# Optimization experiments

Measured on AMD Instinct MI355X. Metric: run time of the kernel, lower is better.

## Reference

```python
import jax, jax.numpy as jnp
import numpy as np

T = 6   # n_tokens_per_window
H = 4   # num_heads


def setup_inputs() -> dict:
    key = jax.random.key(0)
    ks = jax.random.split(key, 13)
    B, N, E = 64, 512, 256
    s = 0.05  # small init scale for weight matrices (stability)
    return {
        "x": jax.random.normal(ks[0], (B, N * T, E), jnp.float32),
        "mask": jax.random.randint(ks[1], (B, N * T), 0, 2, jnp.int32),
        "query": jax.random.normal(ks[2], (E,), jnp.float32),  # classification_query (1,1,E) squeezed
        "in_proj_w": jax.random.normal(ks[3], (3 * E, E), jnp.float32) * s,
        "in_proj_b": jnp.zeros((3 * E,), jnp.float32),
        "out_w": jax.random.normal(ks[4], (E, E), jnp.float32) * s,
        "out_b": jnp.zeros((E,), jnp.float32),
        "ln_g": jnp.ones((E,), jnp.float32),
        "ln_b": jnp.zeros((E,), jnp.float32),
        "w1": jax.random.normal(ks[5], (E // 2, E), jnp.float32) * s,
        "b1": jnp.zeros((E // 2,), jnp.float32),
        "w2": jax.random.normal(ks[6], (1, E // 2), jnp.float32) * s,
        "b2": jnp.zeros((1,), jnp.float32),
    }


def reference(x, mask, query, in_proj_w, in_proj_b, out_w, out_b,
              ln_g, ln_b, w1, b1, w2, b2):
    B, S, E = x.shape
    N = S // T
    BN = B * N
    hd = E // H

    xr = x.reshape(BN, T, E)                      # (BN, T, E)
    mr = mask.reshape(BN, T).astype(bool)         # token validity per window
    valid = mr.any(axis=1)                        # (BN,) window validity

    # --- single-query multi-head attention (torch MHA, eval mode) ---
    Wq, Wk, Wv = in_proj_w[:E], in_proj_w[E:2 * E], in_proj_w[2 * E:]
    bq, bk, bv = in_proj_b[:E], in_proj_b[E:2 * E], in_proj_b[2 * E:]
    q = (query @ Wq.T + bq).reshape(H, hd)        # shared learnable query
    k = (xr @ Wk.T + bk).reshape(BN, T, H, hd)
    v = (xr @ Wv.T + bv).reshape(BN, T, H, hd)

    scores = jnp.einsum('hd,bthd->bht', q, k) / np.float32(np.sqrt(hd))
    scores = jnp.where(mr[:, None, :], scores, jnp.float32(-1e9))  # key_padding_mask
    attw = jax.nn.softmax(scores, axis=-1)        # (BN, H, T)
    attn = jnp.einsum('bht,bthd->bhd', attw, v).reshape(BN, E)
    attn = attn @ out_w.T + out_b                 # out_proj

    # --- classifier: LayerNorm -> Linear -> GELU -> Linear ---
    mu = attn.mean(-1, keepdims=True)
    var = ((attn - mu) ** 2).mean(-1, keepdims=True)
    h = (attn - mu) / jnp.sqrt(var + 1e-5) * ln_g + ln_b
    h = jax.nn.gelu(h @ w1.T + b1, approximate=False)
    logits = h @ w2.T + b2                        # (BN, 1)

    # zero-fill fully masked windows (torch: logits[~valid_windows_mask] = 0)
    logits = jnp.where(valid[:, None], logits, jnp.float32(0.0))
    return logits.reshape(B, N)                   # n_classes == 1 -> squeeze
```

## Files before the change

kernel.cpp:

```cpp
#include <hip/hip_runtime.h>
#include <math.h>

#define TT 6
#define HH 4
#define EE 256
#define RB 16
#define PR 8
#define NTHREADS 256

typedef __attribute__((ext_vector_type(8))) short bf16x8;
typedef __attribute__((ext_vector_type(4))) float f32x4;

__device__ __forceinline__ unsigned short f2b(float f) {
    union { float f; unsigned u; } v; v.f = f;
    unsigned u = v.u + 0x7fffu + ((v.u >> 16) & 1u);
    return (unsigned short)(u >> 16);
}
__device__ __forceinline__ float b2f(unsigned short s) {
    union { unsigned u; float f; } v; v.u = ((unsigned)s) << 16;
    return v.f;
}

#define SWT_OFF 0
#define SB_OFF  8192
#define Q_OFF   8208
#define WVB_OFF 9232
#define OWB_OFF 140304
#define W1B_OFF 271376

__global__ void setup_q(const float* __restrict__ query,
                        const float* __restrict__ in_proj_w,
                        const float* __restrict__ in_proj_b,
                        unsigned char* __restrict__ ws)
{
    __shared__ float qs[EE];
    float* qv = (float*)(ws + Q_OFF);
    float* sb = (float*)(ws + SB_OFF);
    const int tid = threadIdx.x;
    float acc = in_proj_b[tid];
    const float* row = in_proj_w + (size_t)tid * EE;
    for (int e = 0; e < EE; e += 4) {
        float4 w = *(const float4*)(row + e);
        float4 q = *(const float4*)(query + e);
        acc += w.x * q.x + w.y * q.y + w.z * q.z + w.w * q.w;
    }
    qs[tid] = acc;
    qv[tid] = acc;
    __syncthreads();
    if (tid < HH) {
        float a = 0.f;
        for (int d = 0; d < 64; ++d) a += qs[tid * 64 + d] * in_proj_b[EE + tid * 64 + d];
        sb[tid] = a;
    }
}

__global__ void setup_cast(const float* __restrict__ in_proj_w,
                           const float* __restrict__ out_w,
                           const float* __restrict__ w1,
                           unsigned char* __restrict__ ws)
{
    unsigned short* swt = (unsigned short*)(ws + SWT_OFF);
    const float*    qv  = (const float*)(ws + Q_OFF);
    unsigned short* wvb = (unsigned short*)(ws + WVB_OFF);
    unsigned short* owb = (unsigned short*)(ws + OWB_OFF);
    unsigned short* w1b = (unsigned short*)(ws + W1B_OFF);

    const int tid = threadIdx.x;
    const int gidx = blockIdx.x * NTHREADS + tid;
    const int gstride = gridDim.x * NTHREADS;

    for (int i = gidx; i < 65536; i += gstride) wvb[i] = f2b(in_proj_w[512 * 256 + i]);
    for (int i = gidx; i < 65536; i += gstride) owb[i] = f2b(out_w[i]);
    for (int i = gidx; i < 32768; i += gstride) w1b[i] = f2b(w1[i]);

    if (blockIdx.x < HH) {
        const int n = blockIdx.x;
        float a = 0.f;
        for (int d = 0; d < 64; ++d)
            a += qv[n * 64 + d] * in_proj_w[(size_t)(EE + n * 64 + d) * EE + tid];
        swt[n * EE + tid] = f2b(a);
    } else if (blockIdx.x == HH) {
        for (int i = HH * EE + tid; i < 16 * EE; i += NTHREADS) swt[i] = 0;
    }
}

#define XS_OFF   0
#define XBT_OFF  24960
#define SCF_OFF  57856
#define AW_OFF   58816
#define VAL_OFF  59584
#define MB_OFF   59648
#define POOL_SZ  59840
#define YB_OFF   0
#define OUTV_OFF 8320
#define LNB_OFF  0
#define HB_OFF   8320

__global__ __launch_bounds__(NTHREADS, 2)
void fused_head_kernel(const float* __restrict__ x,
                       const int* __restrict__ mask,
                       const float* __restrict__ in_proj_b,
                       const float* __restrict__ out_b,
                       const float* __restrict__ ln_g,
                       const float* __restrict__ ln_b,
                       const float* __restrict__ b1,
                       const float* __restrict__ w2,
                       const float* __restrict__ b2,
                       const unsigned char* __restrict__ ws,
                       float* __restrict__ out)
{
    __shared__ __align__(16) unsigned char pool[POOL_SZ];
    unsigned short* xs   = (unsigned short*)(pool + XS_OFF);
    unsigned short* xbt  = (unsigned short*)(pool + XBT_OFF);
    float*          scf  = (float*)(pool + SCF_OFF);
    float*          aw4  = (float*)(pool + AW_OFF);
    float*          vldf = (float*)(pool + VAL_OFF);
    int*            mbuf = (int*)(pool + MB_OFF);
    unsigned short* yb   = (unsigned short*)(pool + YB_OFF);
    float*          outv = (float*)(pool + OUTV_OFF);
    unsigned short* lnb  = (unsigned short*)(pool + LNB_OFF);
    unsigned short* hb   = (unsigned short*)(pool + HB_OFF);

    const unsigned short* swt = (const unsigned short*)(ws + SWT_OFF);
    const float*          sb  = (const float*)(ws + SB_OFF);
    const unsigned short* wvb = (const unsigned short*)(ws + WVB_OFF);
    const unsigned short* owb = (const unsigned short*)(ws + OWB_OFF);
    const unsigned short* w1b = (const unsigned short*)(ws + W1B_OFF);

    const int tid = threadIdx.x;
    const int wv  = tid >> 6;
    const int ln  = tid & 63;
    const int qd  = ln >> 4;
    const int nl  = ln & 15;
    const int chunk0 = blockIdx.x * RB;

    for (int p = 0; p < 2; ++p) {
        const int c0 = chunk0 + p * PR;
        __syncthreads();
        if (tid < PR * TT) mbuf[tid] = mask[(size_t)c0 * TT + tid];
        const float* xp = x + (size_t)c0 * (TT * EE);
        for (int i = 0; i < 12; ++i) {
            int f = i * 1024 + tid * 4;
            float4 v = *(const float4*)(xp + f);
            int r = f >> 8, e = f & 255;
            union { unsigned short u[4]; uint2 v2; } t2;
            t2.u[0] = f2b(v.x); t2.u[1] = f2b(v.y);
            t2.u[2] = f2b(v.z); t2.u[3] = f2b(v.w);
            *(uint2*)(xs + r * 260 + e) = t2.v2;
        }
        __syncthreads();
        if (wv < 3) {
            const int mt = wv;
            f32x4 acc = {0.f, 0.f, 0.f, 0.f};
            for (int kb = 0; kb < EE; kb += 32) {
                bf16x8 a = *(const bf16x8*)(xs + (mt * 16 + nl) * 260 + kb + qd * 8);
                bf16x8 b = *(const bf16x8*)(swt + nl * EE + kb + qd * 8);
                acc = __builtin_amdgcn_mfma_f32_16x16x32_bf16(a, b, acc, 0, 0, 0);
            }
            if (nl < HH) {
#pragma unroll
                for (int i = 0; i < 4; ++i)
                    scf[(mt * 16 + qd * 4 + i) * 5 + nl] = acc[i];
            }
        }
        __syncthreads();
        if (tid < PR * HH) {
            int g = tid >> 2, h = tid & 3;
            const int* mrow = mbuf + g * TT;
            float sbh = sb[h];
            float vs[TT]; float m = -1e30f;
#pragma unroll
            for (int t = 0; t < TT; ++t) {
                float s = scf[(g * TT + t) * 5 + h] * 0.125f + sbh;
                s = mrow[t] ? s : -1e9f;
                vs[t] = s; m = fmaxf(m, s);
            }
            float sum = 0.f;
#pragma unroll
            for (int t = 0; t < TT; ++t) { float e = __expf(vs[t] - m); vs[t] = e; sum += e; }
            float inv = 1.f / sum;
#pragma unroll
            for (int t = 0; t < TT; ++t) aw4[(g * TT + t) * 4 + h] = vs[t] * inv;
            if (h == 0) {
                int vvv = 0;
#pragma unroll
                for (int t = 0; t < TT; ++t) vvv |= mrow[t];
                vldf[p * PR + g] = vvv ? 1.f : 0.f;
            }
        }
        __syncthreads();
        {
            const int e  = (tid & 127) * 2;
            const int g0 = (tid >> 7) * 4;
            for (int gi = 0; gi < 4; ++gi) {
                int g = g0 + gi;
                float a0[HH] = {0.f, 0.f, 0.f, 0.f};
                float a1[HH] = {0.f, 0.f, 0.f, 0.f};
#pragma unroll
                for (int t = 0; t < TT; ++t) {
                    unsigned xp2 = *(const unsigned*)(xs + (g * TT + t) * 260 + e);
                    float x0 = b2f((unsigned short)(xp2 & 0xffffu));
                    float x1 = b2f((unsigned short)(xp2 >> 16));
                    float4 a = *(const float4*)(aw4 + (g * TT + t) * 4);
                    a0[0] += a.x * x0; a0[1] += a.y * x0; a0[2] += a.z * x0; a0[3] += a.w * x0;
                    a1[0] += a.x * x1; a1[1] += a.y * x1; a1[2] += a.z * x1; a1[3] += a.w * x1;
                }
                int grow = p * PR + g;
#pragma unroll
                for (int h = 0; h < HH; ++h) {
                    unsigned pk = (unsigned)f2b(a0[h]) | ((unsigned)f2b(a1[h]) << 16);
                    *(unsigned*)(xbt + grow * 1028 + h * EE + e) = pk;
                }
            }
        }
    }
    __syncthreads();

    {
        const int h = wv;
        f32x4 acc[4];
#pragma unroll
        for (int nt = 0; nt < 4; ++nt) acc[nt] = (f32x4){0.f, 0.f, 0.f, 0.f};
        for (int kb = 0; kb < EE; kb += 32) {
            bf16x8 a = *(const bf16x8*)(xbt + nl * 1028 + h * EE + kb + qd * 8);
#pragma unroll
            for (int nt = 0; nt < 4; ++nt) {
                int j = h * 64 + nt * 16 + nl;
                bf16x8 b = *(const bf16x8*)(wvb + (size_t)j * EE + kb + qd * 8);
                acc[nt] = __builtin_amdgcn_mfma_f32_16x16x32_bf16(a, b, acc[nt], 0, 0, 0);
            }
        }
#pragma unroll
        for (int nt = 0; nt < 4; ++nt) {
            int j = h * 64 + nt * 16 + nl;
            float bvj = in_proj_b[2 * EE + j];
#pragma unroll
            for (int i = 0; i < 4; ++i)
                yb[(qd * 4 + i) * 260 + j] = f2b(acc[nt][i] + bvj);
        }
    }
    __syncthreads();

    {
        f32x4 acc[4];
#pragma unroll
        for (int nt = 0; nt < 4; ++nt) acc[nt] = (f32x4){0.f, 0.f, 0.f, 0.f};
        for (int kb = 0; kb < EE; kb += 32) {
            bf16x8 a = *(const bf16x8*)(yb + nl * 260 + kb + qd * 8);
#pragma unroll
            for (int nt = 0; nt < 4; ++nt) {
                int j = wv * 64 + nt * 16 + nl;
                bf16x8 b = *(const bf16x8*)(owb + (size_t)j * EE + kb + qd * 8);
                acc[nt] = __builtin_amdgcn_mfma_f32_16x16x32_bf16(a, b, acc[nt], 0, 0, 0);
            }
        }
#pragma unroll
        for (int nt = 0; nt < 4; ++nt) {
            int j = wv * 64 + nt * 16 + nl;
            float obj = out_b[j];
#pragma unroll
            for (int i = 0; i < 4; ++i)
                outv[(qd * 4 + i) * 260 + j] = acc[nt][i] + obj;
        }
    }
    __syncthreads();

    {
        int g = tid >> 4, kc = tid & 15;
        float vals[16];
        float s = 0.f, ss = 0.f;
#pragma unroll
        for (int i = 0; i < 4; ++i) {
            float4 v = *(const float4*)(outv + g * 260 + kc * 16 + i * 4);
            vals[i * 4 + 0] = v.x; vals[i * 4 + 1] = v.y;
            vals[i * 4 + 2] = v.z; vals[i * 4 + 3] = v.w;
            s += v.x + v.y + v.z + v.w;
            ss += v.x * v.x + v.y * v.y + v.z * v.z + v.w * v.w;
        }
#pragma unroll
        for (int d = 8; d; d >>= 1) { s += __shfl_xor(s, d, 64); ss += __shfl_xor(ss, d, 64); }
        float mu = s * (1.f / EE);
        float var = ss * (1.f / EE) - mu * mu;
        float rstd = rsqrtf(var + 1e-5f);
#pragma unroll
        for (int i = 0; i < 16; i += 2) {
            int j = kc * 16 + i;
            float2 gg = *(const float2*)(ln_g + j);
            float2 bb = *(const float2*)(ln_b + j);
            float o0 = (vals[i]     - mu) * rstd * gg.x + bb.x;
            float o1 = (vals[i + 1] - mu) * rstd * gg.y + bb.y;
            unsigned pk = (unsigned)f2b(o0) | ((unsigned)f2b(o1) << 16);
            *(unsigned*)(lnb + g * 260 + j) = pk;
        }
    }
    __syncthreads();

    {
        f32x4 acc[2];
#pragma unroll
        for (int nt = 0; nt < 2; ++nt) acc[nt] = (f32x4){0.f, 0.f, 0.f, 0.f};
        for (int kb = 0; kb < EE; kb += 32) {
            bf16x8 a = *(const bf16x8*)(lnb + nl * 260 + kb + qd * 8);
#pragma unroll
            for (int nt = 0; nt < 2; ++nt) {
                int j = wv * 32 + nt * 16 + nl;
                bf16x8 b = *(const bf16x8*)(w1b + (size_t)j * EE + kb + qd * 8);
                acc[nt] = __builtin_amdgcn_mfma_f32_16x16x32_bf16(a, b, acc[nt], 0, 0, 0);
            }
        }
#pragma unroll
        for (int nt = 0; nt < 2; ++nt) {
            int j = wv * 32 + nt * 16 + nl;
            float bj = b1[j];
#pragma unroll
            for (int i = 0; i < 4; ++i) {
                float sv = acc[nt][i] + bj;
                float ge = 0.5f * sv * (1.0f + erff(sv * 0.70710678118654752f));
                hb[(qd * 4 + i) * 136 + j] = f2b(ge);
            }
        }
    }
    __syncthreads();

    {
        int g = tid >> 4, j0 = (tid & 15) * 8;
        float part = 0.f;
#pragma unroll
        for (int i = 0; i < 8; i += 2) {
            unsigned pk = *(const unsigned*)(hb + g * 136 + j0 + i);
            float h0 = b2f((unsigned short)(pk & 0xffffu));
            float h1 = b2f((unsigned short)(pk >> 16));
            float2 ww = *(const float2*)(w2 + j0 + i);
            part += ww.x * h0 + ww.y * h1;
        }
#pragma unroll
        for (int d = 8; d; d >>= 1) part += __shfl_xor(part, d, 64);
        if ((tid & 15) == 0) out[chunk0 + g] = (part + b2[0]) * vldf[g];
    }
}

extern "C" void kernel_launch(void* const* d_in, const int* in_sizes, int n_in,
                              void* d_out, int out_size, void* d_ws, size_t ws_size,
                              hipStream_t stream) {
    const float* x         = (const float*)d_in[0];
    const int*   mask      = (const int*)d_in[1];
    const float* query     = (const float*)d_in[2];
    const float* in_proj_w = (const float*)d_in[3];
    const float* in_proj_b = (const float*)d_in[4];
    const float* out_w     = (const float*)d_in[5];
    const float* out_b     = (const float*)d_in[6];
    const float* ln_g      = (const float*)d_in[7];
    const float* ln_b      = (const float*)d_in[8];
    const float* w1        = (const float*)d_in[9];
    const float* b1        = (const float*)d_in[10];
    const float* w2        = (const float*)d_in[11];
    const float* b2        = (const float*)d_in[12];
    float* out = (float*)d_out;
    unsigned char* ws = (unsigned char*)d_ws;

    const int BN = out_size;

    setup_q<<<1, NTHREADS, 0, stream>>>(query, in_proj_w, in_proj_b, ws);
    setup_cast<<<128, NTHREADS, 0, stream>>>(in_proj_w, out_w, w1, ws);
    fused_head_kernel<<<BN / RB, NTHREADS, 0, stream>>>(
        x, mask, in_proj_b, out_b, ln_g, ln_b, b1, w2, b2, ws, out);
}
```

Before: 394.8 us.

## Split fused head into attention and MLP kernels via workspace intermediate

The single fused kernel is split in two. The first computes attention pooling per 8 windows with small shared memory and writes bf16 pooled head vectors to the global workspace. The second runs the value projection, out projection, LayerNorm and MLP per wave with register-held accumulators and fewer block syncs, and the two setup kernels are merged into one. The aim is higher occupancy and more MFMA work per wave, at the cost of an extra global round trip (BN×1024 bf16) and a dependence on workspace size for slicing.

```diff
diff --git a/kernel.cpp b/kernel.cpp
--- a/kernel.cpp
+++ b/kernel.cpp
@@ -4,8 +4,6 @@
 #define TT 6
 #define HH 4
 #define EE 256
-#define RB 16
-#define PR 8
 #define NTHREADS 256
 
 typedef __attribute__((ext_vector_type(8))) short bf16x8;
@@ -23,44 +21,21 @@
 
 #define SWT_OFF 0
 #define SB_OFF  8192
-#define Q_OFF   8208
-#define WVB_OFF 9232
-#define OWB_OFF 140304
-#define W1B_OFF 271376
-
-__global__ void setup_q(const float* __restrict__ query,
-                        const float* __restrict__ in_proj_w,
-                        const float* __restrict__ in_proj_b,
-                        unsigned char* __restrict__ ws)
-{
-    __shared__ float qs[EE];
-    float* qv = (float*)(ws + Q_OFF);
-    float* sb = (float*)(ws + SB_OFF);
-    const int tid = threadIdx.x;
-    float acc = in_proj_b[tid];
-    const float* row = in_proj_w + (size_t)tid * EE;
-    for (int e = 0; e < EE; e += 4) {
-        float4 w = *(const float4*)(row + e);
-        float4 q = *(const float4*)(query + e);
-        acc += w.x * q.x + w.y * q.y + w.z * q.z + w.w * q.w;
-    }
-    qs[tid] = acc;
-    qv[tid] = acc;
-    __syncthreads();
-    if (tid < HH) {
-        float a = 0.f;
-        for (int d = 0; d < 64; ++d) a += qs[tid * 64 + d] * in_proj_b[EE + tid * 64 + d];
-        sb[tid] = a;
-    }
-}
-
-__global__ void setup_cast(const float* __restrict__ in_proj_w,
-                           const float* __restrict__ out_w,
-                           const float* __restrict__ w1,
-                           unsigned char* __restrict__ ws)
+#define WVB_OFF 8208
+#define OWB_OFF 139280
+#define W1B_OFF 270352
+#define VLD_OFF 335888
+#define XB_OFF  466960
+
+__global__ void setup_all(const float* __restrict__ query,
+                          const float* __restrict__ in_proj_w,
+                          const float* __restrict__ in_proj_b,
+                          const float* __restrict__ out_w,
+                          const float* __restrict__ w1,
+                          unsigned char* __restrict__ ws)
 {
     unsigned short* swt = (unsigned short*)(ws + SWT_OFF);
-    const float*    qv  = (const float*)(ws + Q_OFF);
+    float*          sb  = (float*)(ws + SB_OFF);
     unsigned short* wvb = (unsigned short*)(ws + WVB_OFF);
     unsigned short* owb = (unsigned short*)(ws + OWB_OFF);
     unsigned short* w1b = (unsigned short*)(ws + W1B_OFF);
@@ -75,70 +50,66 @@
 
     if (blockIdx.x < HH) {
         const int n = blockIdx.x;
-        float a = 0.f;
-        for (int d = 0; d < 64; ++d)
-            a += qv[n * 64 + d] * in_proj_w[(size_t)(EE + n * 64 + d) * EE + tid];
-        swt[n * EE + tid] = f2b(a);
+        __shared__ float qld[64];
+        {
+            int d = tid >> 2, qt = tid & 3;
+            const float* wr = in_proj_w + (size_t)(n * 64 + d) * EE + qt * 64;
+            const float* qr = query + qt * 64;
+            float part = 0.f;
+            for (int e = 0; e < 64; e += 4) {
+                float4 w = *(const float4*)(wr + e);
+                float4 q = *(const float4*)(qr + e);
+                part += w.x * q.x + w.y * q.y + w.z * q.z + w.w * q.w;
+            }
+            part += __shfl_xor(part, 1, 64);
+            part += __shfl_xor(part, 2, 64);
+            if (qt == 0) qld[d] = part + in_proj_b[n * 64 + d];
+        }
+        __syncthreads();
+        {
+            float a = 0.f;
+            for (int d = 0; d < 64; ++d)
+                a += qld[d] * in_proj_w[(size_t)(EE + n * 64 + d) * EE + tid];
+            swt[n * EE + tid] = f2b(a);
+        }
+        if (tid == 0) {
+            float a = 0.f;
+            for (int d = 0; d < 64; ++d) a += qld[d] * in_proj_b[EE + n * 64 + d];
+            sb[n] = a;
+        }
     } else if (blockIdx.x == HH) {
         for (int i = HH * EE + tid; i < 16 * EE; i += NTHREADS) swt[i] = 0;
     }
 }
 
-#define XS_OFF   0
-#define XBT_OFF  24960
-#define SCF_OFF  57856
-#define AW_OFF   58816
-#define VAL_OFF  59584
-#define MB_OFF   59648
-#define POOL_SZ  59840
-#define YB_OFF   0
-#define OUTV_OFF 8320
-#define LNB_OFF  0
-#define HB_OFF   8320
-
-__global__ __launch_bounds__(NTHREADS, 2)
-void fused_head_kernel(const float* __restrict__ x,
-                       const int* __restrict__ mask,
-                       const float* __restrict__ in_proj_b,
-                       const float* __restrict__ out_b,
-                       const float* __restrict__ ln_g,
-                       const float* __restrict__ ln_b,
-                       const float* __restrict__ b1,
-                       const float* __restrict__ w2,
-                       const float* __restrict__ b2,
-                       const unsigned char* __restrict__ ws,
-                       float* __restrict__ out)
+__global__ __launch_bounds__(NTHREADS, 5)
+void k1_attn(const float* __restrict__ x,
+             const int* __restrict__ mask,
+             unsigned char* __restrict__ ws,
+             int s0)
 {
-    __shared__ __align__(16) unsigned char pool[POOL_SZ];
-    unsigned short* xs   = (unsigned short*)(pool + XS_OFF);
-    unsigned short* xbt  = (unsigned short*)(pool + XBT_OFF);
-    float*          scf  = (float*)(pool + SCF_OFF);
-    float*          aw4  = (float*)(pool + AW_OFF);
-    float*          vldf = (float*)(pool + VAL_OFF);
-    int*            mbuf = (int*)(pool + MB_OFF);
-    unsigned short* yb   = (unsigned short*)(pool + YB_OFF);
-    float*          outv = (float*)(pool + OUTV_OFF);
-    unsigned short* lnb  = (unsigned short*)(pool + LNB_OFF);
-    unsigned short* hb   = (unsigned short*)(pool + HB_OFF);
+    __shared__ __align__(16) unsigned short xs[48 * 260];
+    __shared__ float scf[48 * 5];
+    __shared__ float aw4[8 * TT * 4];
+    __shared__ int   mbuf[48];
 
     const unsigned short* swt = (const unsigned short*)(ws + SWT_OFF);
     const float*          sb  = (const float*)(ws + SB_OFF);
-    const unsigned short* wvb = (const unsigned short*)(ws + WVB_OFF);
-    const unsigned short* owb = (const unsigned short*)(ws + OWB_OFF);
-    const unsigned short* w1b = (const unsigned short*)(ws + W1B_OFF);
+    float*                vld = (float*)(ws + VLD_OFF);
+    unsigned*             xbg = (unsigned*)(ws + XB_OFF);
 
     const int tid = threadIdx.x;
     const int wv  = tid >> 6;
     const int ln  = tid & 63;
     const int qd  = ln >> 4;
     const int nl  = ln & 15;
-    const int chunk0 = blockIdx.x * RB;
-
-    for (int p = 0; p < 2; ++p) {
-        const int c0 = chunk0 + p * PR;
-        __syncthreads();
-        if (tid < PR * TT) mbuf[tid] = mask[(size_t)c0 * TT + tid];
+    const int c0  = s0 + blockIdx.x * 8;
+    const int r0  = blockIdx.x * 8;
+
+    if (tid < 48) mbuf[tid] = mask[(size_t)c0 * TT + tid];
+    {
         const float* xp = x + (size_t)c0 * (TT * EE);
+#pragma unroll
         for (int i = 0; i < 12; ++i) {
             int f = i * 1024 + tid * 4;
             float4 v = *(const float4*)(xp + f);
@@ -148,194 +119,227 @@
             t2.u[2] = f2b(v.z); t2.u[3] = f2b(v.w);
             *(uint2*)(xs + r * 260 + e) = t2.v2;
         }
-        __syncthreads();
-        if (wv < 3) {
-            const int mt = wv;
-            f32x4 acc = {0.f, 0.f, 0.f, 0.f};
-            for (int kb = 0; kb < EE; kb += 32) {
-                bf16x8 a = *(const bf16x8*)(xs + (mt * 16 + nl) * 260 + kb + qd * 8);
-                bf16x8 b = *(const bf16x8*)(swt + nl * EE + kb + qd * 8);
-                acc = __builtin_amdgcn_mfma_f32_16x16x32_bf16(a, b, acc, 0, 0, 0);
-            }
-            if (nl < HH) {
-#pragma unroll
-                for (int i = 0; i < 4; ++i)
-                    scf[(mt * 16 + qd * 4 + i) * 5 + nl] = acc[i];
-            }
-        }
-        __syncthreads();
-        if (tid < PR * HH) {
-            int g = tid >> 2, h = tid & 3;
-            const int* mrow = mbuf + g * TT;
-            float sbh = sb[h];
-            float vs[TT]; float m = -1e30f;
+    }
+    __syncthreads();
+    if (wv < 3) {
+        const int mt = wv;
+        f32x4 acc = {0.f, 0.f, 0.f, 0.f};
+        for (int kb = 0; kb < EE; kb += 32) {
+            bf16x8 a = *(const bf16x8*)(xs + (mt * 16 + nl) * 260 + kb + qd * 8);
+            bf16x8 b = *(const bf16x8*)(swt + nl * EE + kb + qd * 8);
+            acc = __builtin_amdgcn_mfma_f32_16x16x32_bf16(a, b, acc, 0, 0, 0);
+        }
+        if (nl < HH) {
+#pragma unroll
+            for (int i = 0; i < 4; ++i)
+                scf[(mt * 16 + qd * 4 + i) * 5 + nl] = acc[i];
+        }
+    }
+    __syncthreads();
+    if (tid < 32) {
+        int g = tid >> 2, h = tid & 3;
+        const int* mrow = mbuf + g * TT;
+        float sbh = sb[h];
+        float vs[TT]; float m = -1e30f;
+#pragma unroll
+        for (int t = 0; t < TT; ++t) {
+            float s = scf[(g * TT + t) * 5 + h] * 0.125f + sbh;
+            s = mrow[t] ? s : -1e9f;
+            vs[t] = s; m = fmaxf(m, s);
+        }
+        float sum = 0.f;
+#pragma unroll
+        for (int t = 0; t < TT; ++t) { float e = __expf(vs[t] - m); vs[t] = e; sum += e; }
+        float inv = 1.f / sum;
+#pragma unroll
+        for (int t = 0; t < TT; ++t) aw4[(g * TT + t) * 4 + h] = vs[t] * inv;
+        if (h == 0) {
+            int vvv = 0;
+#pragma unroll
+            for (int t = 0; t < TT; ++t) vvv |= mrow[t];
+            vld[c0 + g] = vvv ? 1.f : 0.f;
+        }
+    }
+    __syncthreads();
+    {
+        const int e  = (tid & 127) * 2;
+        const int g0 = (tid >> 7) * 4;
+        for (int gi = 0; gi < 4; ++gi) {
+            int g = g0 + gi;
+            float a0[HH] = {0.f, 0.f, 0.f, 0.f};
+            float a1[HH] = {0.f, 0.f, 0.f, 0.f};
 #pragma unroll
             for (int t = 0; t < TT; ++t) {
-                float s = scf[(g * TT + t) * 5 + h] * 0.125f + sbh;
-                s = mrow[t] ? s : -1e9f;
-                vs[t] = s; m = fmaxf(m, s);
-            }
-            float sum = 0.f;
-#pragma unroll
-            for (int t = 0; t < TT; ++t) { float e = __expf(vs[t] - m); vs[t] = e; sum += e; }
-            float inv = 1.f / sum;
-#pragma unroll
-            for (int t = 0; t < TT; ++t) aw4[(g * TT + t) * 4 + h] = vs[t] * inv;
-            if (h == 0) {
-                int vvv = 0;
-#pragma unroll
-                for (int t = 0; t < TT; ++t) vvv |= mrow[t];
-                vldf[p * PR + g] = vvv ? 1.f : 0.f;
-            }
-        }
-        __syncthreads();
-        {
-            const int e  = (tid & 127) * 2;
-            const int g0 = (tid >> 7) * 4;
-            for (int gi = 0; gi < 4; ++gi) {
-                int g = g0 + gi;
-                float a0[HH] = {0.f, 0.f, 0.f, 0.f};
-                float a1[HH] = {0.f, 0.f, 0.f, 0.f};
-#pragma unroll
-                for (int t = 0; t < TT; ++t) {
-                    unsigned xp2 = *(const unsigned*)(xs + (g * TT + t) * 260 + e);
-                    float x0 = b2f((unsigned short)(xp2 & 0xffffu));
-                    float x1 = b2f((unsigned short)(xp2 >> 16));
-                    float4 a = *(const float4*)(aw4 + (g * TT + t) * 4);
-                    a0[0] += a.x * x0; a0[1] += a.y * x0; a0[2] += a.z * x0; a0[3] += a.w * x0;
-                    a1[0] += a.x * x1; a1[1] += a.y * x1; a1[2] += a.z * x1; a1[3] += a.w * x1;
+                unsigned xp2 = *(const unsigned*)(xs + (g * TT + t) * 260 + e);
+                float x0 = b2f((unsigned short)(xp2 & 0xffffu));
+                float x1 = b2f((unsigned short)(xp2 >> 16));
+                float4 a = *(const float4*)(aw4 + (g * TT + t) * 4);
+                a0[0] += a.x * x0; a0[1] += a.y * x0; a0[2] += a.z * x0; a0[3] += a.w * x0;
+                a1[0] += a.x * x1; a1[1] += a.y * x1; a1[2] += a.z * x1; a1[3] += a.w * x1;
+            }
+            size_t row = (size_t)(r0 + g) * 512;
+#pragma unroll
+            for (int h = 0; h < HH; ++h) {
+                unsigned pk = (unsigned)f2b(a0[h]) | ((unsigned)f2b(a1[h]) << 16);
+                xbg[row + h * 128 + (e >> 1)] = pk;
+            }
+        }
+    }
+}
+
+__global__ __launch_bounds__(NTHREADS, 3)
+void k2_head(const float* __restrict__ in_proj_b,
+             const float* __restrict__ out_b,
+             const float* __restrict__ ln_g,
+             const float* __restrict__ ln_b,
+             const float* __restrict__ b1,
+             const float* __restrict__ w2,
+             const float* __restrict__ b2,
+             const unsigned char* __restrict__ ws,
+             int s0,
+             float* __restrict__ out)
+{
+    __shared__ __align__(16) unsigned short ybuf[4][16 * 264];
+
+    const unsigned short* xbg = (const unsigned short*)(ws + XB_OFF);
+    const unsigned short* wvb = (const unsigned short*)(ws + WVB_OFF);
+    const unsigned short* owb = (const unsigned short*)(ws + OWB_OFF);
+    const unsigned short* w1b = (const unsigned short*)(ws + W1B_OFF);
+    const float*          vld = (const float*)(ws + VLD_OFF);
+
+    const int tid = threadIdx.x;
+    const int wv  = tid >> 6;
+    const int ln  = tid & 63;
+    const int qd  = ln >> 4;
+    const int nl  = ln & 15;
+    const int lr0 = blockIdx.x * 64 + wv * 16;
+    const int gc0 = s0 + lr0;
+    unsigned short* yw = ybuf[wv];
+
+    {
+        f32x4 acc[16];
+#pragma unroll
+        for (int u = 0; u < 16; ++u) acc[u] = (f32x4){0.f, 0.f, 0.f, 0.f};
+        for (int h = 0; h < HH; ++h) {
+            for (int kb = 0; kb < 8; ++kb) {
+                bf16x8 a = *(const bf16x8*)(xbg + (size_t)(lr0 + nl) * 1024 + h * 256 + kb * 32 + qd * 8);
+#pragma unroll
+                for (int nt = 0; nt < 4; ++nt) {
+                    int j = h * 64 + nt * 16 + nl;
+                    bf16x8 b = *(const bf16x8*)(wvb + (size_t)j * EE + kb * 32 + qd * 8);
+                    acc[h * 4 + nt] = __builtin_amdgcn_mfma_f32_16x16x32_bf16(a, b, acc[h * 4 + nt], 0, 0, 0);
                 }
-                int grow = p * PR + g;
-#pragma unroll
-                for (int h = 0; h < HH; ++h) {
-                    unsigned pk = (unsigned)f2b(a0[h]) | ((unsigned)f2b(a1[h]) << 16);
-                    *(unsigned*)(xbt + grow * 1028 + h * EE + e) = pk;
-                }
-            }
-        }
-    }
-    __syncthreads();
-
-    {
-        const int h = wv;
-        f32x4 acc[4];
-#pragma unroll
-        for (int nt = 0; nt < 4; ++nt) acc[nt] = (f32x4){0.f, 0.f, 0.f, 0.f};
-        for (int kb = 0; kb < EE; kb += 32) {
-            bf16x8 a = *(const bf16x8*)(xbt + nl * 1028 + h * EE + kb + qd * 8);
-#pragma unroll
-            for (int nt = 0; nt < 4; ++nt) {
-                int j = h * 64 + nt * 16 + nl;
-                bf16x8 b = *(const bf16x8*)(wvb + (size_t)j * EE + kb + qd * 8);
-                acc[nt] = __builtin_amdgcn_mfma_f32_16x16x32_bf16(a, b, acc[nt], 0, 0, 0);
-            }
-        }
-#pragma unroll
-        for (int nt = 0; nt < 4; ++nt) {
-            int j = h * 64 + nt * 16 + nl;
-            float bvj = in_proj_b[2 * EE + j];
+            }
+        }
+#pragma unroll
+        for (int u = 0; u < 16; ++u) {
+            int j = u * 16 + nl;
+            float bv = in_proj_b[2 * EE + j];
 #pragma unroll
             for (int i = 0; i < 4; ++i)
-                yb[(qd * 4 + i) * 260 + j] = f2b(acc[nt][i] + bvj);
-        }
-    }
-    __syncthreads();
-
-    {
-        f32x4 acc[4];
-#pragma unroll
-        for (int nt = 0; nt < 4; ++nt) acc[nt] = (f32x4){0.f, 0.f, 0.f, 0.f};
-        for (int kb = 0; kb < EE; kb += 32) {
-            bf16x8 a = *(const bf16x8*)(yb + nl * 260 + kb + qd * 8);
-#pragma unroll
-            for (int nt = 0; nt < 4; ++nt) {
-                int j = wv * 64 + nt * 16 + nl;
-                bf16x8 b = *(const bf16x8*)(owb + (size_t)j * EE + kb + qd * 8);
-                acc[nt] = __builtin_amdgcn_mfma_f32_16x16x32_bf16(a, b, acc[nt], 0, 0, 0);
-            }
-        }
-#pragma unroll
-        for (int nt = 0; nt < 4; ++nt) {
-            int j = wv * 64 + nt * 16 + nl;
-            float obj = out_b[j];
-#pragma unroll
-            for (int i = 0; i < 4; ++i)
-                outv[(qd * 4 + i) * 260 + j] = acc[nt][i] + obj;
-        }
-    }
-    __syncthreads();
-
-    {
-        int g = tid >> 4, kc = tid & 15;
-        float vals[16];
-        float s = 0.f, ss = 0.f;
+                yw[(qd * 4 + i) * 264 + j] = f2b(acc[u][i] + bv);
+        }
+    }
+
+    float val[16][4];
+    {
+        f32x4 acc[16];
+#pragma unroll
+        for (int u = 0; u < 16; ++u) acc[u] = (f32x4){0.f, 0.f, 0.f, 0.f};
+        for (int kb = 0; kb < 8; ++kb) {
+            bf16x8 a = *(const bf16x8*)(yw + nl * 264 + kb * 32 + qd * 8);
+#pragma unroll
+            for (int u = 0; u < 16; ++u) {
+                bf16x8 b = *(const bf16x8*)(owb + (size_t)(u * 16 + nl) * EE + kb * 32 + qd * 8);
+                acc[u] = __builtin_amdgcn_mfma_f32_16x16x32_bf16(a, b, acc[u], 0, 0, 0);
+            }
+        }
+#pragma unroll
+        for (int u = 0; u < 16; ++u) {
+            float ob = out_b[u * 16 + nl];
+#pragma unroll
+            for (int i = 0; i < 4; ++i) val[u][i] = acc[u][i] + ob;
+        }
+    }
+
+    {
+        float s[4] = {0.f, 0.f, 0.f, 0.f}, ss[4] = {0.f, 0.f, 0.f, 0.f};
+#pragma unroll
+        for (int u = 0; u < 16; ++u)
+#pragma unroll
+            for (int i = 0; i < 4; ++i) { s[i] += val[u][i]; ss[i] += val[u][i] * val[u][i]; }
+#pragma unroll
+        for (int d = 1; d <= 8; d <<= 1) {
+#pragma unroll
+            for (int i = 0; i < 4; ++i) {
+                s[i]  += __shfl_xor(s[i], d, 64);
+                ss[i] += __shfl_xor(ss[i], d, 64);
+            }
+        }
+        float mu[4], rstd[4];
 #pragma unroll
         for (int i = 0; i < 4; ++i) {
-            float4 v = *(const float4*)(outv + g * 260 + kc * 16 + i * 4);
-            vals[i * 4 + 0] = v.x; vals[i * 4 + 1] = v.y;
-            vals[i * 4 + 2] = v.z; vals[i * 4 + 3] = v.w;
-            s += v.x + v.y + v.z + v.w;
-            ss += v.x * v.x + v.y * v.y + v.z * v.z + v.w * v.w;
-        }
-#pragma unroll
-        for (int d = 8; d; d >>= 1) { s += __shfl_xor(s, d, 64); ss += __shfl_xor(ss, d, 64); }
-        float mu = s * (1.f / EE);
-        float var = ss * (1.f / EE) - mu * mu;
-        float rstd = rsqrtf(var + 1e-5f);
-#pragma unroll
-        for (int i = 0; i < 16; i += 2) {
-            int j = kc * 16 + i;
-            float2 gg = *(const float2*)(ln_g + j);
-            float2 bb = *(const float2*)(ln_b + j);
-            float o0 = (vals[i]     - mu) * rstd * gg.x + bb.x;
-            float o1 = (vals[i + 1] - mu) * rstd * gg.y + bb.y;
-            unsigned pk = (unsigned)f2b(o0) | ((unsigned)f2b(o1) << 16);
-            *(unsigned*)(lnb + g * 260 + j) = pk;
-        }
-    }
-    __syncthreads();
-
-    {
-        f32x4 acc[2];
-#pragma unroll
-        for (int nt = 0; nt < 2; ++nt) acc[nt] = (f32x4){0.f, 0.f, 0.f, 0.f};
-        for (int kb = 0; kb < EE; kb += 32) {
-            bf16x8 a = *(const bf16x8*)(lnb + nl * 260 + kb + qd * 8);
-#pragma unroll
-            for (int nt = 0; nt < 2; ++nt) {
-                int j = wv * 32 + nt * 16 + nl;
-                bf16x8 b = *(const bf16x8*)(w1b + (size_t)j * EE + kb + qd * 8);
-                acc[nt] = __builtin_amdgcn_mfma_f32_16x16x32_bf16(a, b, acc[nt], 0, 0, 0);
-            }
-        }
-#pragma unroll
-        for (int nt = 0; nt < 2; ++nt) {
-            int j = wv * 32 + nt * 16 + nl;
-            float bj = b1[j];
+            mu[i] = s[i] * (1.f / EE);
+            float var = ss[i] * (1.f / EE) - mu[i] * mu[i];
+            rstd[i] = rsqrtf(var + 1e-5f);
+        }
+#pragma unroll
+        for (int u = 0; u < 16; ++u) {
+            int j = u * 16 + nl;
+            float gg = ln_g[j], bb = ln_b[j];
 #pragma unroll
             for (int i = 0; i < 4; ++i) {
-                float sv = acc[nt][i] + bj;
-                float ge = 0.5f * sv * (1.0f + erff(sv * 0.70710678118654752f));
-                hb[(qd * 4 + i) * 136 + j] = f2b(ge);
-            }
-        }
-    }
-    __syncthreads();
-
-    {
-        int g = tid >> 4, j0 = (tid & 15) * 8;
-        float part = 0.f;
-#pragma unroll
-        for (int i = 0; i < 8; i += 2) {
-            unsigned pk = *(const unsigned*)(hb + g * 136 + j0 + i);
-            float h0 = b2f((unsigned short)(pk & 0xffffu));
-            float h1 = b2f((unsigned short)(pk >> 16));
-            float2 ww = *(const float2*)(w2 + j0 + i);
-            part += ww.x * h0 + ww.y * h1;
-        }
-#pragma unroll
-        for (int d = 8; d; d >>= 1) part += __shfl_xor(part, d, 64);
-        if ((tid & 15) == 0) out[chunk0 + g] = (part + b2[0]) * vldf[g];
+                float o = (val[u][i] - mu[i]) * rstd[i] * gg + bb;
+                yw[(qd * 4 + i) * 264 + j] = f2b(o);
+            }
+        }
+    }
+
+    float ge[8][4];
+    {
+        f32x4 acc[8];
+#pragma unroll
+        for (int u = 0; u < 8; ++u) acc[u] = (f32x4){0.f, 0.f, 0.f, 0.f};
+        for (int kb = 0; kb < 8; ++kb) {
+            bf16x8 a = *(const bf16x8*)(yw + nl * 264 + kb * 32 + qd * 8);
+#pragma unroll
+            for (int u = 0; u < 8; ++u) {
+                bf16x8 b = *(const bf16x8*)(w1b + (size_t)(u * 16 + nl) * EE + kb * 32 + qd * 8);
+                acc[u] = __builtin_amdgcn_mfma_f32_16x16x32_bf16(a, b, acc[u], 0, 0, 0);
+            }
+        }
+#pragma unroll
+        for (int u = 0; u < 8; ++u) {
+            float bj = b1[u * 16 + nl];
+#pragma unroll
+            for (int i = 0; i < 4; ++i) {
+                float sv = acc[u][i] + bj;
+                ge[u][i] = 0.5f * sv * (1.0f + erff(sv * 0.70710678118654752f));
+            }
+        }
+    }
+
+    {
+        float w2v[8];
+#pragma unroll
+        for (int u = 0; u < 8; ++u) w2v[u] = w2[u * 16 + nl];
+        float part[4] = {0.f, 0.f, 0.f, 0.f};
+#pragma unroll
+        for (int u = 0; u < 8; ++u)
+#pragma unroll
+            for (int i = 0; i < 4; ++i) part[i] += ge[u][i] * w2v[u];
+#pragma unroll
+        for (int d = 1; d <= 8; d <<= 1)
+#pragma unroll
+            for (int i = 0; i < 4; ++i) part[i] += __shfl_xor(part[i], d, 64);
+        if (nl == 0) {
+            float bb = b2[0];
+#pragma unroll
+            for (int i = 0; i < 4; ++i) {
+                int c = gc0 + qd * 4 + i;
+                out[c] = (part[i] + bb) * vld[c];
+            }
+        }
     }
 }
 
@@ -360,8 +364,18 @@
 
     const int BN = out_size;
 
-    setup_q<<<1, NTHREADS, 0, stream>>>(query, in_proj_w, in_proj_b, ws);
-    setup_cast<<<128, NTHREADS, 0, stream>>>(in_proj_w, out_w, w1, ws);
-    fused_head_kernel<<<BN / RB, NTHREADS, 0, stream>>>(
-        x, mask, in_proj_b, out_b, ln_g, ln_b, b1, w2, b2, ws, out);
-}
+    setup_all<<<128, NTHREADS, 0, stream>>>(query, in_proj_w, in_proj_b, out_w, w1, ws);
+
+    size_t cap_bytes = ws_size > (size_t)XB_OFF ? ws_size - (size_t)XB_OFF : 0;
+    int cap = (int)(cap_bytes / (size_t)(EE * HH * 2));
+    int slice = (cap >= BN) ? BN : (cap / 64) * 64;
+    if (slice < 64) slice = 64;
+    if (slice > BN) slice = BN;
+
+    for (int sbase = 0; sbase < BN; sbase += slice) {
+        int sc = BN - sbase < slice ? BN - sbase : slice;
+        k1_attn<<<sc / 8, NTHREADS, 0, stream>>>(x, mask, ws, sbase);
+        k2_head<<<sc / 64, NTHREADS, 0, stream>>>(in_proj_b, out_b, ln_g, ln_b,
+                                                  b1, w2, b2, ws, sbase, out);
+    }
+}
```

Result: slower. 413.9 us (+4.8%).
